# Optimization experiments

Measured on AMD Instinct MI355X. Metric: run time of the kernel, lower is better.

## Reference

```python
import jax, jax.numpy as jnp
import numpy as np

B = 32768   # batch
D = 1024    # input_dimension
H = 2048    # hidden width (layer_sizes = [2048, 2048])
LN_EPS = 1e-5


def _layer_norm(h, g, b):
    m = jnp.mean(h, axis=-1, keepdims=True)
    v = jnp.var(h, axis=-1, keepdims=True)
    return (h - m) * jax.lax.rsqrt(v + LN_EPS) * g + b


def setup_inputs() -> dict:
    key = jax.random.key(0)
    ks = jax.random.split(key, 5)
    s1 = 1.0 / np.sqrt(D)
    s2 = 1.0 / np.sqrt(H)
    return {
        "x": jax.random.normal(ks[0], (B, D), dtype=jnp.float32),
        "W1": jax.random.uniform(ks[1], (D, H), jnp.float32, -s1, s1),
        "b1": jax.random.uniform(ks[2], (H,), jnp.float32, -s1, s1),
        "g1": jnp.ones((H,), jnp.float32),
        "be1": jnp.zeros((H,), jnp.float32),
        "W2": jax.random.uniform(ks[3], (H, 9), jnp.float32, -s2, s2),
        "b2": jax.random.uniform(ks[4], (9,), jnp.float32, -s2, s2),
        "g2": jnp.ones((9,), jnp.float32),
        "be2": jnp.zeros((9,), jnp.float32),
    }


def reference(x, W1, b1, g1, be1, W2, b2, g2, be2):
    # MLP: Linear -> ReLU -> LayerNorm, twice (final width 9)
    h = _layer_norm(jax.nn.relu(x @ W1 + b1), g1, be1)      # [B, H]
    r = _layer_norm(jax.nn.relu(h @ W2 + b2), g2, be2)      # [B, 9]
    R = r.reshape(x.shape[0], 3, 3)                          # [B, 3, 3]
    # SVD projection onto SO(3): U @ diag(1,1,det(U Vh)) @ Vh
    U, _, Vh = jnp.linalg.svd(R, full_matrices=False)
    d = jnp.linalg.det(U @ Vh)                               # [B]
    scale = jnp.stack([jnp.ones_like(d), jnp.ones_like(d), d], axis=-1)  # [B,3]
    return (U * scale[:, None, :]) @ Vh                      # scale last col of U
```

## Files before the change

### kernel.cpp

```cpp
#include <hip/hip_runtime.h>

typedef unsigned short u16;
typedef _Float16 f16x8 __attribute__((ext_vector_type(8)));
typedef unsigned short us8 __attribute__((ext_vector_type(8)));
typedef float f32x4 __attribute__((ext_vector_type(4)));

#define GLD16(gptr, lptr)                                                              \
  __builtin_amdgcn_global_load_lds((const __attribute__((address_space(1))) void*)(gptr), \
                                   (__attribute__((address_space(3))) void*)(lptr), 16, 0, 0)

#define MFMA_F16(a, b, c) __builtin_amdgcn_mfma_f32_16x16x32_f16((a), (b), (c), 0, 0, 0)

__global__ __launch_bounds__(256) void k_split_x(const float* __restrict__ x,
                                                 u16* __restrict__ xh, u16* __restrict__ xl) {
  size_t i = (size_t)blockIdx.x * 256 + threadIdx.x;
  const float4* xf = (const float4*)x;
  float4 a = xf[2 * i], b = xf[2 * i + 1];
  float vv[8] = {a.x, a.y, a.z, a.w, b.x, b.y, b.z, b.w};
  f16x8 H, L;
#pragma unroll
  for (int j = 0; j < 8; ++j) {
    _Float16 hi = (_Float16)vv[j];
    H[j] = hi;
    L[j] = (_Float16)(vv[j] - (float)hi);
  }
  const int row = (int)(i >> 7);
  const int qp = ((int)i & 3) ^ ((row >> 1) & 3);
  const size_t dst = (i & ~(size_t)3) | (size_t)qp;
  *(f16x8*)(xh + dst * 8) = H;
  *(f16x8*)(xl + dst * 8) = L;
}

__global__ __launch_bounds__(256) void k_split_w1t(const float* __restrict__ w1,
                                                   u16* __restrict__ wh, u16* __restrict__ wl) {
  __shared__ float tile[32][33];
  int bn = blockIdx.x & 63;
  int bk = blockIdx.x >> 6;
  int tn = threadIdx.x & 31, tq = threadIdx.x >> 5;
#pragma unroll
  for (int r = 0; r < 4; ++r) {
    int k = bk * 32 + tq + r * 8;
    tile[tq + r * 8][tn] = w1[(size_t)k * 2048 + bn * 32 + tn];
  }
  __syncthreads();
#pragma unroll
  for (int r = 0; r < 4; ++r) {
    int n = bn * 32 + tq + r * 8;
    float v = tile[tn][tq + r * 8];
    _Float16 hi = (_Float16)v;
    _Float16 lo = (_Float16)(v - (float)hi);
    int qp = (tn >> 3) ^ ((n >> 1) & 3);
    int kp = bk * 32 + qp * 8 + (tn & 7);
    wh[(size_t)n * 1024 + kp] = __builtin_bit_cast(u16, hi);
    wl[(size_t)n * 1024 + kp] = __builtin_bit_cast(u16, lo);
  }
}

__global__ __launch_bounds__(256) void k_w2frag(const float* __restrict__ w2, const float* __restrict__ g1,
                                                u16* __restrict__ fh, u16* __restrict__ fl) {
  int t = blockIdx.x * 256 + threadIdx.x;
  int c = t >> 6, l = t & 63;
  int col = l & 15, lg = l >> 4;
  f16x8 H, L;
#pragma unroll
  for (int j = 0; j < 8; ++j) {
    int k = c * 32 + lg * 8 + j;
    float v = (col < 9) ? g1[k] * w2[k * 9 + col] : 0.f;
    _Float16 hi = (_Float16)v;
    H[j] = hi;
    L[j] = (_Float16)(v - (float)hi);
  }
  *(f16x8*)(fh + (size_t)t * 8) = H;
  *(f16x8*)(fl + (size_t)t * 8) = L;
}

__global__ void k_cgcb(const float* __restrict__ w2, const float* __restrict__ g1,
                       const float* __restrict__ be1, double* __restrict__ cgcb) {
  int l = threadIdx.x;
  double cg[9], cb[9];
#pragma unroll
  for (int j = 0; j < 9; ++j) { cg[j] = 0.0; cb[j] = 0.0; }
  for (int i = 0; i < 32; ++i) {
    int k = i * 64 + l;
    double g = (double)g1[k], b = (double)be1[k];
#pragma unroll
    for (int j = 0; j < 9; ++j) {
      double w = (double)w2[k * 9 + j];
      cg[j] += g * w;
      cb[j] += b * w;
    }
  }
  for (int off = 32; off; off >>= 1) {
#pragma unroll
    for (int j = 0; j < 9; ++j) {
      cg[j] += __shfl_xor(cg[j], off, 64);
      cb[j] += __shfl_xor(cb[j], off, 64);
    }
  }
  if (l == 0) {
    for (int j = 0; j < 16; ++j) {
      cgcb[j] = (j < 9) ? cg[j] : 0.0;
      cgcb[16 + j] = (j < 9) ? cb[j] : 0.0;
    }
  }
}

__global__ __launch_bounds__(512, 2) void k_gemm1(const u16* __restrict__ xh, const u16* __restrict__ xl,
                                                  const u16* __restrict__ wh, const u16* __restrict__ wl,
                                                  const float* __restrict__ b1,
                                                  const u16* __restrict__ fh, const u16* __restrict__ fl,
                                                  float* __restrict__ pdot, float* __restrict__ pstat) {
  __shared__ __align__(16) u16 lds[2][4][8192];
  const int tid = threadIdx.x;
  const int swz = ((blockIdx.x & 7) << 7) | (blockIdx.x >> 3);
  const int m0 = (swz >> 3) << 8;
  const int n0 = (swz & 7) << 8;
  const int lane = tid & 63, w = tid >> 6;
  const int wr = (w >> 2) << 7;
  const int wc = (w & 3) << 6;
  const int lr = lane & 15, lg = lane >> 4;

  int a_off[8], b_off[4];
#pragma unroll
  for (int i = 0; i < 8; ++i) {
    int row = wr + i * 16 + lr;
    a_off[i] = row * 32 + ((lg ^ ((row >> 1) & 3)) << 3);
  }
#pragma unroll
  for (int j = 0; j < 4; ++j) {
    int row = wc + j * 16 + lr;
    b_off[j] = row * 32 + ((lg ^ ((row >> 1) & 3)) << 3);
  }

  const size_t aoff = (size_t)(m0 + (tid >> 2)) * 1024 + ((tid & 3) << 3);
  const size_t boff = (size_t)(n0 + (tid >> 2)) * 1024 + ((tid & 3) << 3);

#define STAGE1(bf, mt, src, off, kk)                          \
  do {                                                        \
    GLD16((src) + (off) + (kk), &lds[bf][mt][tid * 8]);       \
    GLD16((src) + (off) + 131072 + (kk), &lds[bf][mt][4096 + tid * 8]); \
  } while (0)

  STAGE1(0, 0, xh, aoff, 0);
  STAGE1(0, 1, xl, aoff, 0);
  STAGE1(0, 2, wh, boff, 0);
  STAGE1(0, 3, wl, boff, 0);

  f32x4 acc[8][4] = {};
#pragma unroll 2
  for (int kt = 0; kt < 32; ++kt) {
    const int cur = kt & 1, nxt = cur ^ 1;
    const int nk = (kt < 31 ? kt + 1 : 31) * 32;
    STAGE1(nxt, 0, xh, aoff, nk);
    asm volatile("s_waitcnt vmcnt(2)" ::: "memory");
    __builtin_amdgcn_s_barrier();
    asm volatile("" ::: "memory");
    const u16* Ah = &lds[cur][0][0];
    const u16* Al = &lds[cur][1][0];
    const u16* Bh = &lds[cur][2][0];
    const u16* Bl = &lds[cur][3][0];
    f16x8 bhf[4], blf[4], ahf[4], alf[4];

#define RD_B(j)                                         \
  do {                                                  \
    bhf[j] = *(const f16x8*)(Bh + b_off[j]);            \
    blf[j] = *(const f16x8*)(Bl + b_off[j]);            \
  } while (0)
#define RD_A(s, i)                                      \
  do {                                                  \
    ahf[s] = *(const f16x8*)(Ah + a_off[i]);            \
    alf[s] = *(const f16x8*)(Al + a_off[i]);            \
  } while (0)
#define MM(s, i, j)                                     \
  do {                                                  \
    acc[i][j] = MFMA_F16(ahf[s], bhf[j], acc[i][j]);    \
    acc[i][j] = MFMA_F16(ahf[s], blf[j], acc[i][j]);    \
    acc[i][j] = MFMA_F16(alf[s], bhf[j], acc[i][j]);    \
  } while (0)
#define PRIO1 __builtin_amdgcn_s_setprio(1)
#define PRIO0 __builtin_amdgcn_s_setprio(0)

    RD_B(0); RD_A(0, 0);
    PRIO1; MM(0, 0, 0); PRIO0;
    RD_A(1, 1);
    PRIO1; MM(1, 1, 0); PRIO0;
    RD_B(1);
    STAGE1(nxt, 1, xl, aoff, nk);
    PRIO1; MM(0, 0, 1); MM(1, 1, 1); PRIO0;
    RD_A(2, 2);
    PRIO1; MM(2, 2, 0); MM(2, 2, 1); PRIO0;
    RD_A(3, 3);
    PRIO1; MM(3, 3, 0); MM(3, 3, 1); PRIO0;
    RD_B(2);
    STAGE1(nxt, 2, wh, boff, nk);
    PRIO1; MM(0, 0, 2); MM(1, 1, 2); MM(2, 2, 2); MM(3, 3, 2); PRIO0;
    RD_B(3);
    PRIO1; MM(0, 0, 3); MM(1, 1, 3); MM(2, 2, 3); MM(3, 3, 3); PRIO0;
    RD_A(0, 4);
    STAGE1(nxt, 3, wl, boff, nk);
    PRIO1; MM(0, 4, 0); MM(0, 4, 1); MM(0, 4, 2); MM(0, 4, 3); PRIO0;
    RD_A(1, 5);
    PRIO1; MM(1, 5, 0); MM(1, 5, 1); MM(1, 5, 2); MM(1, 5, 3); PRIO0;
    RD_A(2, 6);
    PRIO1; MM(2, 6, 0); MM(2, 6, 1); MM(2, 6, 2); MM(2, 6, 3); PRIO0;
    RD_A(3, 7);
    PRIO1; MM(3, 7, 0); MM(3, 7, 1); MM(3, 7, 2); MM(3, 7, 3); PRIO0;
#undef RD_B
#undef RD_A
#undef MM
#undef PRIO1
#undef PRIO0
    asm volatile("" ::: "memory");
    __builtin_amdgcn_s_barrier();
  }
#undef STAGE1

  asm volatile("s_waitcnt vmcnt(0)" ::: "memory");
  __syncthreads();
  float* vt = (float*)&lds[0][0][0];

#pragma unroll
  for (int j = 0; j < 4; ++j) {
    const float bias = b1[n0 + wc + j * 16 + lr];
#pragma unroll
    for (int i = 0; i < 8; ++i)
#pragma unroll
      for (int r = 0; r < 4; ++r) acc[i][j][r] = fmaxf(acc[i][j][r] + bias, 0.f);
  }

  f32x4 acc2[2] = {};
  float sstat[2] = {0.f, 0.f}, qstat[2] = {0.f, 0.f};
  const int myrow0 = w * 32;

#pragma unroll
  for (int half = 0; half < 2; ++half) {
    if (((w & 3) >> 1) == half) {
      const int colbase = wc & 127;
#pragma unroll
      for (int j = 0; j < 4; ++j) {
        const int lcol = colbase + j * 16 + lr;
        const int g = lcol >> 2, wsel = lcol & 3;
#pragma unroll
        for (int i = 0; i < 8; ++i)
#pragma unroll
          for (int r = 0; r < 4; ++r) {
            const int row = wr + i * 16 + lg * 4 + r;
            vt[row * 128 + ((g ^ (row & 7)) << 2) + wsel] = acc[i][j][r];
          }
      }
    }
    __syncthreads();
#pragma unroll
    for (int cl = 0; cl < 4; ++cl) {
      const int cglob = (n0 >> 5) + half * 4 + cl;
      const f16x8 bh = *(const f16x8*)(fh + (size_t)(cglob * 64 + lane) * 8);
      const f16x8 bl = *(const f16x8*)(fl + (size_t)(cglob * 64 + lane) * 8);
#pragma unroll
      for (int g2 = 0; g2 < 2; ++g2) {
        const int row = myrow0 + g2 * 16 + lr;
        const int g0 = cl * 8 + lg * 2;
        const float4 f0 = *(const float4*)&vt[row * 128 + ((g0 ^ (row & 7)) << 2)];
        const float4 f1 = *(const float4*)&vt[row * 128 + (((g0 + 1) ^ (row & 7)) << 2)];
        float f[8] = {f0.x, f0.y, f0.z, f0.w, f1.x, f1.y, f1.z, f1.w};
        f16x8 AH, AL;
#pragma unroll
        for (int e = 0; e < 8; ++e) {
          sstat[g2] += f[e];
          qstat[g2] = fmaf(f[e], f[e], qstat[g2]);
          _Float16 hi = (_Float16)f[e];
          AH[e] = hi;
          AL[e] = (_Float16)(f[e] - (float)hi);
        }
        acc2[g2] = MFMA_F16(AH, bh, acc2[g2]);
        acc2[g2] = MFMA_F16(AH, bl, acc2[g2]);
        acc2[g2] = MFMA_F16(AL, bh, acc2[g2]);
      }
    }
    __syncthreads();
  }

#pragma unroll
  for (int g2 = 0; g2 < 2; ++g2) {
    sstat[g2] += __shfl_xor(sstat[g2], 16, 64);
    sstat[g2] += __shfl_xor(sstat[g2], 32, 64);
    qstat[g2] += __shfl_xor(qstat[g2], 16, 64);
    qstat[g2] += __shfl_xor(qstat[g2], 32, 64);
  }
  const int ntile = n0 >> 8;
#pragma unroll
  for (int g2 = 0; g2 < 2; ++g2) {
    if (lg == 0) {
      const int row = m0 + myrow0 + g2 * 16 + lr;
      *(float2*)&pstat[((size_t)row * 8 + ntile) * 2] = make_float2(sstat[g2], qstat[g2]);
    }
    if (lr < 9) {
#pragma unroll
      for (int r = 0; r < 4; ++r) {
        const int row = m0 + myrow0 + g2 * 16 + lg * 4 + r;
        pdot[((size_t)row * 8 + ntile) * 12 + lr] = acc2[g2][r];
      }
    }
  }
}

static __device__ __forceinline__ void jrot(double S[3][3], double V[3][3], int p, int q, int r) {
  double apq = S[p][q];
  if (apq == 0.0) return;
  double tau = (S[q][q] - S[p][p]) / (2.0 * apq);
  double t = (tau >= 0.0 ? 1.0 : -1.0) / (fabs(tau) + sqrt(1.0 + tau * tau));
  double c = 1.0 / sqrt(1.0 + t * t);
  double s = t * c;
  double spp = S[p][p], sqq = S[q][q];
  double srp = S[r][p], srq = S[r][q];
  S[p][p] = spp - t * apq;
  S[q][q] = sqq + t * apq;
  S[p][q] = 0.0; S[q][p] = 0.0;
  S[r][p] = c * srp - s * srq; S[p][r] = S[r][p];
  S[r][q] = s * srp + c * srq; S[q][r] = S[r][q];
#pragma unroll
  for (int i = 0; i < 3; ++i) {
    double vip = V[i][p], viq = V[i][q];
    V[i][p] = c * vip - s * viq;
    V[i][q] = s * vip + c * viq;
  }
}

static __device__ void svd_so3(const double* Rf, float* Of) {
  double A[3][3], S[3][3];
  double V[3][3] = {{1, 0, 0}, {0, 1, 0}, {0, 0, 1}};
#pragma unroll
  for (int i = 0; i < 3; ++i)
#pragma unroll
    for (int j = 0; j < 3; ++j) A[i][j] = Rf[i * 3 + j];
#pragma unroll
  for (int p = 0; p < 3; ++p)
#pragma unroll
    for (int q = 0; q < 3; ++q) {
      double sa = 0.0;
#pragma unroll
      for (int i = 0; i < 3; ++i) sa += A[i][p] * A[i][q];
      S[p][q] = sa;
    }
  for (int it = 0; it < 6; ++it) {
    jrot(S, V, 0, 1, 2);
    jrot(S, V, 0, 2, 1);
    jrot(S, V, 1, 2, 0);
  }
  double l0 = S[0][0], l1 = S[1][1], l2 = S[2][2];
  double c0[3] = {V[0][0], V[1][0], V[2][0]};
  double c1[3] = {V[0][1], V[1][1], V[2][1]};
  double c2[3] = {V[0][2], V[1][2], V[2][2]};
  double tl, tv;
#define SWP(la, lb, ca, cb)                                         \
  if (la < lb) {                                                    \
    tl = la; la = lb; lb = tl;                                      \
    tv = ca[0]; ca[0] = cb[0]; cb[0] = tv;                          \
    tv = ca[1]; ca[1] = cb[1]; cb[1] = tv;                          \
    tv = ca[2]; ca[2] = cb[2]; cb[2] = tv;                          \
  }
  SWP(l0, l1, c0, c1)
  SWP(l0, l2, c0, c2)
  SWP(l1, l2, c1, c2)
#undef SWP
  double v3[3];
  v3[0] = c0[1] * c1[2] - c0[2] * c1[1];
  v3[1] = c0[2] * c1[0] - c0[0] * c1[2];
  v3[2] = c0[0] * c1[1] - c0[1] * c1[0];
  double t1[3], t2[3];
#pragma unroll
  for (int i = 0; i < 3; ++i) {
    t1[i] = A[i][0] * c0[0] + A[i][1] * c0[1] + A[i][2] * c0[2];
    t2[i] = A[i][0] * c1[0] + A[i][1] * c1[1] + A[i][2] * c1[2];
  }
  double n1 = sqrt(t1[0] * t1[0] + t1[1] * t1[1] + t1[2] * t1[2]);
  if (n1 < 1e-20) {
#pragma unroll
    for (int t = 0; t < 9; ++t) Of[t] = (t == 0 || t == 4 || t == 8) ? 1.f : 0.f;
    return;
  }
  double u1[3], u2[3], u3[3];
  double r1 = 1.0 / n1;
#pragma unroll
  for (int i = 0; i < 3; ++i) u1[i] = t1[i] * r1;
  double d12 = u1[0] * t2[0] + u1[1] * t2[1] + u1[2] * t2[2];
#pragma unroll
  for (int i = 0; i < 3; ++i) t2[i] -= d12 * u1[i];
  double n2 = sqrt(t2[0] * t2[0] + t2[1] * t2[1] + t2[2] * t2[2]);
  if (n2 > 1e-14 * n1) {
    double r2 = 1.0 / n2;
#pragma unroll
    for (int i = 0; i < 3; ++i) u2[i] = t2[i] * r2;
  } else {
    double ax = fabs(u1[0]), ay = fabs(u1[1]), az = fabs(u1[2]);
    double e[3] = {0.0, 0.0, 0.0};
    if (ax <= ay && ax <= az) e[0] = 1.0;
    else if (ay <= az) e[1] = 1.0;
    else e[2] = 1.0;
    double d = e[0] * u1[0] + e[1] * u1[1] + e[2] * u1[2];
#pragma unroll
    for (int i = 0; i < 3; ++i) e[i] -= d * u1[i];
    double nn = 1.0 / sqrt(e[0] * e[0] + e[1] * e[1] + e[2] * e[2]);
#pragma unroll
    for (int i = 0; i < 3; ++i) u2[i] = e[i] * nn;
  }
  u3[0] = u1[1] * u2[2] - u1[2] * u2[1];
  u3[1] = u1[2] * u2[0] - u1[0] * u2[2];
  u3[2] = u1[0] * u2[1] - u1[1] * u2[0];
#pragma unroll
  for (int i = 0; i < 3; ++i)
#pragma unroll
    for (int j = 0; j < 3; ++j)
      Of[i * 3 + j] = (float)(u1[i] * c0[j] + u2[i] * c1[j] + u3[i] * v3[j]);
}

__global__ __launch_bounds__(256) void k_comb(const float* __restrict__ pdot,
                                              const float* __restrict__ pstat,
                                              const double* __restrict__ cgcb,
                                              const float* __restrict__ b2,
                                              const float* __restrict__ g2v,
                                              const float* __restrict__ be2,
                                              float* __restrict__ out) {
  const int row = blockIdx.x * 256 + threadIdx.x;
  double dj[9];
#pragma unroll
  for (int j = 0; j < 9; ++j) dj[j] = 0.0;
  double s = 0.0, q = 0.0;
#pragma unroll
  for (int nt = 0; nt < 8; ++nt) {
    const float* p = pdot + ((size_t)row * 8 + nt) * 12;
#pragma unroll
    for (int j = 0; j < 9; ++j) dj[j] += (double)p[j];
    const float* ps = pstat + ((size_t)row * 8 + nt) * 2;
    s += (double)ps[0];
    q += (double)ps[1];
  }
  const double mean = s * (1.0 / 2048.0);
  const double varr = fmax(q * (1.0 / 2048.0) - mean * mean, 0.0);
  const double inv = 1.0 / sqrt(varr + 1e-5);
  double a2[9];
  double s9 = 0.0, q9 = 0.0;
#pragma unroll
  for (int j = 0; j < 9; ++j) {
    double v = inv * (dj[j] - mean * cgcb[j]) + cgcb[16 + j] + (double)b2[j];
    v = fmax(v, 0.0);
    a2[j] = v;
    s9 += v;
    q9 += v * v;
  }
  const double m2 = s9 * (1.0 / 9.0);
  const double v2c = fmax(q9 * (1.0 / 9.0) - m2 * m2, 0.0);
  const double i2 = 1.0 / sqrt(v2c + 1e-5);
  double rn[9];
#pragma unroll
  for (int j = 0; j < 9; ++j) rn[j] = (a2[j] - m2) * i2 * (double)g2v[j] + (double)be2[j];
  float O[9];
  svd_so3(rn, O);
  float* op = out + (size_t)row * 9;
#pragma unroll
  for (int t = 0; t < 9; ++t) op[t] = O[t];
}

extern "C" void kernel_launch(void* const* d_in, const int* in_sizes, int n_in,
                              void* d_out, int out_size, void* d_ws, size_t ws_size,
                              hipStream_t stream) {
  const float* x   = (const float*)d_in[0];
  const float* W1  = (const float*)d_in[1];
  const float* b1  = (const float*)d_in[2];
  const float* g1  = (const float*)d_in[3];
  const float* be1 = (const float*)d_in[4];
  const float* W2  = (const float*)d_in[5];
  const float* b2  = (const float*)d_in[6];
  const float* g2  = (const float*)d_in[7];
  const float* be2 = (const float*)d_in[8];
  float* out = (float*)d_out;
  char* ws = (char*)d_ws;
  u16*    xh   = (u16*)(ws + 0);
  u16*    xl   = (u16*)(ws + 67108864);
  u16*    wh   = (u16*)(ws + 134217728);
  u16*    wl   = (u16*)(ws + 138412032);
  u16*    fh   = (u16*)(ws + 142606336);
  u16*    fl   = (u16*)(ws + 142671872);
  double* cgcb = (double*)(ws + 142737408);
  float*  pdot = (float*)(ws + 142737664);
  float*  pstat= (float*)(ws + 155320576);

  k_split_x<<<dim3(16384), dim3(256), 0, stream>>>(x, xh, xl);
  k_split_w1t<<<dim3(2048), dim3(256), 0, stream>>>(W1, wh, wl);
  k_w2frag<<<dim3(16), dim3(256), 0, stream>>>(W2, g1, fh, fl);
  k_cgcb<<<dim3(1), dim3(64), 0, stream>>>(W2, g1, be1, cgcb);
  k_gemm1<<<dim3(1024), dim3(512), 0, stream>>>(xh, xl, wh, wl, b1, fh, fl, pdot, pstat);
  k_comb<<<dim3(128), dim3(256), 0, stream>>>(pdot, pstat, cgcb, b2, g2, be2, out);
}
```

Measured before the change: 401.6 us.

## Fuse x fp16 hi/lo split into GEMM1 by loading fp32 x into LDS

Removes the separate k_split_x pass, so the GEMM loads fp32 x tiles directly into LDS with a new swizzle and splits them into fp16 hi/lo fragments in registers just before the MFMAs. This saves the 128MB read plus 128MB write of the split kernel and one launch. In exchange, the conversion work is repeated for each N-tile block (8 times per element), and each A fragment needs extra VALU instructions and two LDS reads inside the MFMA loop, which may compete with matrix issue.

```diff
diff --git a/kernel.cpp b/kernel.cpp
--- a/kernel.cpp
+++ b/kernel.cpp
@@ -2,7 +2,6 @@
 
 typedef unsigned short u16;
 typedef _Float16 f16x8 __attribute__((ext_vector_type(8)));
-typedef unsigned short us8 __attribute__((ext_vector_type(8)));
 typedef float f32x4 __attribute__((ext_vector_type(4)));
 
 #define GLD16(gptr, lptr)                                                              \
@@ -10,26 +9,6 @@
                                    (__attribute__((address_space(3))) void*)(lptr), 16, 0, 0)
 
 #define MFMA_F16(a, b, c) __builtin_amdgcn_mfma_f32_16x16x32_f16((a), (b), (c), 0, 0, 0)
-
-__global__ __launch_bounds__(256) void k_split_x(const float* __restrict__ x,
-                                                 u16* __restrict__ xh, u16* __restrict__ xl) {
-  size_t i = (size_t)blockIdx.x * 256 + threadIdx.x;
-  const float4* xf = (const float4*)x;
-  float4 a = xf[2 * i], b = xf[2 * i + 1];
-  float vv[8] = {a.x, a.y, a.z, a.w, b.x, b.y, b.z, b.w};
-  f16x8 H, L;
-#pragma unroll
-  for (int j = 0; j < 8; ++j) {
-    _Float16 hi = (_Float16)vv[j];
-    H[j] = hi;
-    L[j] = (_Float16)(vv[j] - (float)hi);
-  }
-  const int row = (int)(i >> 7);
-  const int qp = ((int)i & 3) ^ ((row >> 1) & 3);
-  const size_t dst = (i & ~(size_t)3) | (size_t)qp;
-  *(f16x8*)(xh + dst * 8) = H;
-  *(f16x8*)(xl + dst * 8) = L;
-}
 
 __global__ __launch_bounds__(256) void k_split_w1t(const float* __restrict__ w1,
                                                    u16* __restrict__ wh, u16* __restrict__ wl) {
@@ -105,12 +84,12 @@
   }
 }
 
-__global__ __launch_bounds__(512, 2) void k_gemm1(const u16* __restrict__ xh, const u16* __restrict__ xl,
+__global__ __launch_bounds__(512, 2) void k_gemm1(const float* __restrict__ x,
                                                   const u16* __restrict__ wh, const u16* __restrict__ wl,
                                                   const float* __restrict__ b1,
                                                   const u16* __restrict__ fh, const u16* __restrict__ fl,
                                                   float* __restrict__ pdot, float* __restrict__ pstat) {
-  __shared__ __align__(16) u16 lds[2][4][8192];
+  __shared__ __align__(16) u16 lds[2][32768];
   const int tid = threadIdx.x;
   const int swz = ((blockIdx.x & 7) << 7) | (blockIdx.x >> 3);
   const int m0 = (swz >> 3) << 8;
@@ -120,45 +99,52 @@
   const int wc = (w & 3) << 6;
   const int lr = lane & 15, lg = lane >> 4;
 
-  int a_off[8], b_off[4];
+  int a_off0[8], a_off1[8];
 #pragma unroll
   for (int i = 0; i < 8; ++i) {
     int row = wr + i * 16 + lr;
-    a_off[i] = row * 32 + ((lg ^ ((row >> 1) & 3)) << 3);
-  }
+    a_off0[i] = row * 32 + (((2 * lg) ^ (row & 7)) << 2);
+    a_off1[i] = row * 32 + (((2 * lg + 1) ^ (row & 7)) << 2);
+  }
+  int b_off[4];
 #pragma unroll
   for (int j = 0; j < 4; ++j) {
     int row = wc + j * 16 + lr;
     b_off[j] = row * 32 + ((lg ^ ((row >> 1) & 3)) << 3);
   }
 
-  const size_t aoff = (size_t)(m0 + (tid >> 2)) * 1024 + ((tid & 3) << 3);
+  const size_t sA = (size_t)(m0 + (tid >> 3)) * 1024 + ((((tid & 7) ^ ((tid >> 3) & 7))) << 2);
   const size_t boff = (size_t)(n0 + (tid >> 2)) * 1024 + ((tid & 3) << 3);
 
-#define STAGE1(bf, mt, src, off, kk)                          \
+#define STAGE_A(bf, kk)                                       \
   do {                                                        \
-    GLD16((src) + (off) + (kk), &lds[bf][mt][tid * 8]);       \
-    GLD16((src) + (off) + 131072 + (kk), &lds[bf][mt][4096 + tid * 8]); \
+    GLD16(x + sA + (kk),          &lds[bf][tid * 8]);         \
+    GLD16(x + sA + 65536 + (kk),  &lds[bf][4096 + tid * 8]);  \
+    GLD16(x + sA + 131072 + (kk), &lds[bf][8192 + tid * 8]);  \
+    GLD16(x + sA + 196608 + (kk), &lds[bf][12288 + tid * 8]); \
   } while (0)
-
-  STAGE1(0, 0, xh, aoff, 0);
-  STAGE1(0, 1, xl, aoff, 0);
-  STAGE1(0, 2, wh, boff, 0);
-  STAGE1(0, 3, wl, boff, 0);
+#define STAGE_B(bf, rb, src, kk)                                       \
+  do {                                                                 \
+    GLD16((src) + boff + (kk),          &lds[bf][(rb) + tid * 8]);     \
+    GLD16((src) + boff + 131072 + (kk), &lds[bf][(rb) + 4096 + tid * 8]); \
+  } while (0)
+
+  STAGE_A(0, 0);
+  STAGE_B(0, 16384, wh, 0);
+  STAGE_B(0, 24576, wl, 0);
 
   f32x4 acc[8][4] = {};
 #pragma unroll 2
   for (int kt = 0; kt < 32; ++kt) {
     const int cur = kt & 1, nxt = cur ^ 1;
     const int nk = (kt < 31 ? kt + 1 : 31) * 32;
-    STAGE1(nxt, 0, xh, aoff, nk);
-    asm volatile("s_waitcnt vmcnt(2)" ::: "memory");
+    STAGE_A(nxt, nk);
+    asm volatile("s_waitcnt vmcnt(4)" ::: "memory");
     __builtin_amdgcn_s_barrier();
     asm volatile("" ::: "memory");
-    const u16* Ah = &lds[cur][0][0];
-    const u16* Al = &lds[cur][1][0];
-    const u16* Bh = &lds[cur][2][0];
-    const u16* Bl = &lds[cur][3][0];
+    const float* Ax = (const float*)&lds[cur][0];
+    const u16* Bh = &lds[cur][16384];
+    const u16* Bl = &lds[cur][24576];
     f16x8 bhf[4], blf[4], ahf[4], alf[4];
 
 #define RD_B(j)                                         \
@@ -166,10 +152,17 @@
     bhf[j] = *(const f16x8*)(Bh + b_off[j]);            \
     blf[j] = *(const f16x8*)(Bl + b_off[j]);            \
   } while (0)
-#define RD_A(s, i)                                      \
-  do {                                                  \
-    ahf[s] = *(const f16x8*)(Ah + a_off[i]);            \
-    alf[s] = *(const f16x8*)(Al + a_off[i]);            \
+#define RD_A(s, i)                                                    \
+  do {                                                                \
+    float4 fa = *(const float4*)(Ax + a_off0[i]);                     \
+    float4 fb = *(const float4*)(Ax + a_off1[i]);                     \
+    float ff[8] = {fa.x, fa.y, fa.z, fa.w, fb.x, fb.y, fb.z, fb.w};   \
+    _Pragma("unroll")                                                 \
+    for (int e = 0; e < 8; ++e) {                                     \
+      _Float16 hi = (_Float16)ff[e];                                  \
+      ahf[s][e] = hi;                                                 \
+      alf[s][e] = (_Float16)(ff[e] - (float)hi);                      \
+    }                                                                 \
   } while (0)
 #define MM(s, i, j)                                     \
   do {                                                  \
@@ -185,19 +178,18 @@
     RD_A(1, 1);
     PRIO1; MM(1, 1, 0); PRIO0;
     RD_B(1);
-    STAGE1(nxt, 1, xl, aoff, nk);
+    STAGE_B(nxt, 16384, wh, nk);
     PRIO1; MM(0, 0, 1); MM(1, 1, 1); PRIO0;
     RD_A(2, 2);
     PRIO1; MM(2, 2, 0); MM(2, 2, 1); PRIO0;
     RD_A(3, 3);
     PRIO1; MM(3, 3, 0); MM(3, 3, 1); PRIO0;
     RD_B(2);
-    STAGE1(nxt, 2, wh, boff, nk);
+    STAGE_B(nxt, 24576, wl, nk);
     PRIO1; MM(0, 0, 2); MM(1, 1, 2); MM(2, 2, 2); MM(3, 3, 2); PRIO0;
     RD_B(3);
     PRIO1; MM(0, 0, 3); MM(1, 1, 3); MM(2, 2, 3); MM(3, 3, 3); PRIO0;
     RD_A(0, 4);
-    STAGE1(nxt, 3, wl, boff, nk);
     PRIO1; MM(0, 4, 0); MM(0, 4, 1); MM(0, 4, 2); MM(0, 4, 3); PRIO0;
     RD_A(1, 5);
     PRIO1; MM(1, 5, 0); MM(1, 5, 1); MM(1, 5, 2); MM(1, 5, 3); PRIO0;
@@ -213,11 +205,12 @@
     asm volatile("" ::: "memory");
     __builtin_amdgcn_s_barrier();
   }
-#undef STAGE1
+#undef STAGE_A
+#undef STAGE_B
 
   asm volatile("s_waitcnt vmcnt(0)" ::: "memory");
   __syncthreads();
-  float* vt = (float*)&lds[0][0][0];
+  float* vt = (float*)&lds[0][0];
 
 #pragma unroll
   for (int j = 0; j < 4; ++j) {
@@ -474,8 +467,6 @@
   const float* be2 = (const float*)d_in[8];
   float* out = (float*)d_out;
   char* ws = (char*)d_ws;
-  u16*    xh   = (u16*)(ws + 0);
-  u16*    xl   = (u16*)(ws + 67108864);
   u16*    wh   = (u16*)(ws + 134217728);
   u16*    wl   = (u16*)(ws + 138412032);
   u16*    fh   = (u16*)(ws + 142606336);
@@ -484,10 +475,9 @@
   float*  pdot = (float*)(ws + 142737664);
   float*  pstat= (float*)(ws + 155320576);
 
-  k_split_x<<<dim3(16384), dim3(256), 0, stream>>>(x, xh, xl);
   k_split_w1t<<<dim3(2048), dim3(256), 0, stream>>>(W1, wh, wl);
   k_w2frag<<<dim3(16), dim3(256), 0, stream>>>(W2, g1, fh, fl);
   k_cgcb<<<dim3(1), dim3(64), 0, stream>>>(W2, g1, be1, cgcb);
-  k_gemm1<<<dim3(1024), dim3(512), 0, stream>>>(xh, xl, wh, wl, b1, fh, fl, pdot, pstat);
+  k_gemm1<<<dim3(1024), dim3(512), 0, stream>>>(x, wh, wl, b1, fh, fl, pdot, pstat);
   k_comb<<<dim3(128), dim3(256), 0, stream>>>(pdot, pstat, cgcb, b2, g2, be2, out);
 }
```

Measured after the change: 430.0 us. 7.1% more time.
